# Optimization experiments

Hardware: AMD Instinct MI355X
Metric: run time of the kernel (lower is better)

The kernel has to match this reference:

```python
import jax, jax.numpy as jnp
import numpy as np

NEG_INF = -jnp.inf


def setup_inputs() -> dict:
    key = jax.random.key(0)
    ks = jax.random.split(key, 20)
    B, N, M = 8, 1024, 128
    F_OP, F_MA, F_E, OUT, HID = 64, 64, 16, 64, 128
    inp = {
        "x": jax.random.normal(ks[0], (B, N, F_OP), dtype=jnp.float32),
        "y": jax.random.normal(ks[1], (B, M, F_MA), dtype=jnp.float32),
        "z": jax.random.normal(ks[2], (B, N, M, F_E), dtype=jnp.float32),
        "op_adj_in": jax.random.randint(ks[3], (B, N, N), 0, 2, dtype=jnp.int32),
        "ma_adj_in": jax.random.randint(ks[4], (B, N, N), 0, 2, dtype=jnp.int32),
        "op_ma_adj": jax.random.randint(ks[5], (B, N, M), 0, 2, dtype=jnp.int32),
        # learned parameters
        "weight_op": jax.random.normal(ks[6], (F_OP, OUT), dtype=jnp.float32) * 0.1,
        "weight_ma": jax.random.normal(ks[7], (F_MA, OUT), dtype=jnp.float32) * 0.1,
        "weight_edge": jax.random.normal(ks[8], (F_E, OUT), dtype=jnp.float32) * 0.1,
        "attention_op": jax.random.normal(ks[9], (1, 2 * OUT), dtype=jnp.float32) * 0.1,
        "attention_ma": jax.random.normal(ks[10], (1, 3 * OUT), dtype=jnp.float32) * 0.1,
        "w1": jax.random.normal(ks[11], (2 * OUT, HID), dtype=jnp.float32) * 0.1,
        "b1": jnp.zeros((HID,), dtype=jnp.float32),
        "w2": jax.random.normal(ks[12], (HID, HID), dtype=jnp.float32) * 0.1,
        "b2": jnp.zeros((HID,), dtype=jnp.float32),
        "wo": jax.random.normal(ks[13], (HID, OUT), dtype=jnp.float32) * 0.1,
        "bo": jnp.zeros((OUT,), dtype=jnp.float32),
    }
    return inp


def reference(x, y, z, op_adj_in, ma_adj_in, op_ma_adj,
              weight_op, weight_ma, weight_edge, attention_op, attention_ma,
              w1, b1, w2, b2, wo, bo):
    OUT = weight_op.shape[1]
    h = jnp.einsum('bni,io->bno', x, weight_op)  # [B,N,OUT]
    # all_combinations[b,i,j] = cat(h[b,j], h[b,i]); dot with attention_op splits:
    a1 = attention_op[0, :OUT]
    a2 = attention_op[0, OUT:]
    e_op = (h @ a2)[:, :, None] + (h @ a1)[:, None, :]  # [B,N,N]
    e_op = jax.nn.leaky_relu(e_op, negative_slope=0.01)

    adj = (jnp.swapaxes(op_adj_in, 1, 2) + op_adj_in
           + jnp.swapaxes(ma_adj_in, 1, 2) + ma_adj_in)  # [B,N,N]
    row_mask = jnp.all(op_ma_adj == 0, axis=-1)  # [B,N] ops with no machine link
    adj = jnp.where(row_mask[:, :, None], 1, adj)
    att = jnp.where(adj > 0, e_op, NEG_INF)
    attention_in_op = jax.nn.softmax(att, axis=2)
    h_prime_op = jnp.einsum('bij,bjo->bio', attention_in_op, h)  # [B,N,OUT]

    h_ma = jnp.einsum('bmi,io->bmo', y, weight_ma)  # [B,M,OUT]
    h_edge = jnp.einsum('bnmi,io->bnmo', z, weight_edge)  # [B,N,M,OUT]
    # cat([h_op_i, h_ma_j, h_edge_ij]) @ attention_ma split into three dots
    am1 = attention_ma[0, :OUT]
    am2 = attention_ma[0, OUT:2 * OUT]
    am3 = attention_ma[0, 2 * OUT:]
    e_ma = (h @ am1)[:, :, None] + (h_ma @ am2)[:, None, :] + h_edge @ am3  # [B,N,M]
    e_ma = jax.nn.leaky_relu(e_ma, negative_slope=0.01)

    adj2 = jnp.where(row_mask[:, :, None], 1, op_ma_adj)
    att2 = jnp.where(adj2 > 0, e_ma, NEG_INF)
    attention_in_ma = jax.nn.softmax(att2, axis=2)  # [B,N,M]
    h_ma_edge = h_ma[:, None, :, :] + h_edge  # [B,N,M,OUT]
    h_prime_ma = jnp.einsum('bnm,bnmo->bno', attention_in_ma, h_ma_edge) + h

    h_prime = jnp.concatenate([h_prime_op, h_prime_ma], axis=-1)  # [B,N,2*OUT]
    embed = jax.nn.elu(h_prime @ w1 + b1)
    embed = jax.nn.elu(embed @ w2 + b2)
    embed = embed @ wo + bo
    embed = jnp.where(row_mask[:, :, None], 0.0, embed)
    return embed
```

## Files before the change

### kernel.cpp

```cpp
#include <hip/hip_runtime.h>
#include <math.h>

#define BB 8
#define NN 1024
#define MM 128
#define FOUT 64
#define HIDN 128

#define OFF_H       0
#define OFF_HMA     524288
#define OFF_HA1     589824
#define OFF_HA2     598016
#define OFF_HAM1    606208
#define OFF_HMAAM2  614400
#define OFF_RMASK   615424
#define OFF_WAM3    623616
#define OFF_HPRIME  623632
#define OFF_RDIR    1672208
#define OFF_OPMB    1934352
#define OFF_WT1HI   1967120
#define OFF_WT1LO   1975312
#define OFF_WT2HI   1983504
#define OFF_WT2LO   1991696
#define OFF_WTOHI   1999888
#define OFF_WTOLO   2003984
#define OFF_HTHI    2008080
#define OFF_HTLO    2270224
#define OFF_HMATHI  2532368
#define OFF_HMATLO  2565136
#define OFF_TRM     2597904

typedef __attribute__((ext_vector_type(8))) short bf16x8;
typedef __attribute__((ext_vector_type(8))) unsigned short u16x8;
typedef __attribute__((ext_vector_type(4))) float f32x4;

__device__ __forceinline__ void splitbf(float v, unsigned short& h, unsigned short& l) {
    unsigned u = __float_as_uint(v);
    unsigned hb = (u + 0x7FFFu + ((u >> 16) & 1u)) >> 16;
    float hf = __uint_as_float(hb << 16);
    float lf = v - hf;
    unsigned ul = __float_as_uint(lf);
    unsigned lb = (ul + 0x7FFFu + ((ul >> 16) & 1u)) >> 16;
    h = (unsigned short)hb; l = (unsigned short)lb;
}

__device__ __forceinline__ unsigned short tobf(float v) {
    unsigned u = __float_as_uint(v);
    return (unsigned short)((u + 0x7FFFu + ((u >> 16) & 1u)) >> 16);
}

__global__ __launch_bounds__(256) void k1_prep(
    const float* __restrict__ x, const float* __restrict__ y,
    const int* __restrict__ op_ma_adj,
    const int* __restrict__ op_adj, const int* __restrict__ ma_adj,
    const float* __restrict__ w_op, const float* __restrict__ w_ma,
    const float* __restrict__ w_edge,
    const float* __restrict__ att_op, const float* __restrict__ att_ma,
    const float* __restrict__ w1_g, const float* __restrict__ w2_g,
    const float* __restrict__ wo_g,
    float* __restrict__ h, float* __restrict__ h_ma,
    float* __restrict__ ha1, float* __restrict__ ha2, float* __restrict__ ham1,
    float* __restrict__ hmaam2, int* __restrict__ rmask, float* __restrict__ wam3,
    unsigned long long* __restrict__ rowdir, unsigned long long* __restrict__ opmb,
    unsigned short* __restrict__ trm,
    unsigned short* __restrict__ wt1hi, unsigned short* __restrict__ wt1lo,
    unsigned short* __restrict__ wt2hi, unsigned short* __restrict__ wt2lo,
    unsigned short* __restrict__ wtohi, unsigned short* __restrict__ wtolo,
    unsigned short* __restrict__ hthi, unsigned short* __restrict__ htlo,
    unsigned short* __restrict__ hmathi, unsigned short* __restrict__ hmatlo)
{
    __shared__ float wlds[64 * 64];
    __shared__ unsigned hstage[8 * 64];
    int bid = blockIdx.x;
    int t = threadIdx.x;
    int lane = t & 63;
    int wv = t >> 6;

    if (bid < 1024) {
        int b = bid >> 7;
        int n0g = (bid & 127) * 8;
        for (int k = t; k < 4096; k += 256) wlds[k] = w_op[k];
        float a1c = att_op[lane], a2c = att_op[64 + lane], am1c = att_ma[lane];
        __syncthreads();
        #pragma unroll
        for (int p = 0; p < 2; ++p) {
            int row = b * NN + n0g + p * 4 + wv;
            float xv = x[(size_t)row * 64 + lane];
            float acc0 = 0.f, acc1 = 0.f, acc2 = 0.f, acc3 = 0.f;
            #pragma unroll
            for (int i = 0; i < 16; ++i) {
                acc0 += __shfl(xv, i)      * wlds[i * 64 + lane];
                acc1 += __shfl(xv, i + 16) * wlds[(i + 16) * 64 + lane];
                acc2 += __shfl(xv, i + 32) * wlds[(i + 32) * 64 + lane];
                acc3 += __shfl(xv, i + 48) * wlds[(i + 48) * 64 + lane];
            }
            float acc = (acc0 + acc1) + (acc2 + acc3);
            h[(size_t)row * 64 + lane] = acc;
            unsigned short hs, ls;
            splitbf(acc, hs, ls);
            hstage[(p * 4 + wv) * 64 + lane] = (unsigned)hs | ((unsigned)ls << 16);
            float d1 = acc * a1c, d2 = acc * a2c, d3 = acc * am1c;
            #pragma unroll
            for (int m = 32; m; m >>= 1) {
                d1 += __shfl_xor(d1, m);
                d2 += __shfl_xor(d2, m);
                d3 += __shfl_xor(d3, m);
            }
            int v0 = op_ma_adj[(size_t)row * 128 + lane];
            int v1 = op_ma_adj[(size_t)row * 128 + 64 + lane];
            unsigned long long w0 = __ballot(v0 != 0);
            unsigned long long w1 = __ballot(v1 != 0);
            if (lane == 0) {
                ha1[row] = d1; ha2[row] = d2; ham1[row] = d3;
                opmb[row * 2] = w0; opmb[row * 2 + 1] = w1;
                rmask[row] = ((w0 | w1) == 0ULL) ? 1 : 0;
            }
        }
        __syncthreads();
        if (t < 128) {
            int o = t & 63;
            int plane = t >> 6;
            int sh = plane * 16;
            unsigned short* dst = plane ? htlo : hthi;
            u16x8 pk;
            #pragma unroll
            for (int k = 0; k < 8; ++k)
                pk[k] = (unsigned short)((hstage[k * 64 + o] >> sh) & 0xFFFFu);
            *(u16x8*)&dst[((size_t)(b * 64 + o)) * 1024 + n0g] = pk;
        }
    } else if (bid < 1152) {
        int bb = (bid - 1024) >> 4;
        int m0 = ((bid - 1024) & 15) * 8;
        for (int k = t; k < 4096; k += 256) wlds[k] = w_ma[k];
        float am2c = att_ma[64 + lane];
        __syncthreads();
        #pragma unroll
        for (int p = 0; p < 2; ++p) {
            int row = bb * MM + m0 + p * 4 + wv;
            float yv = y[(size_t)row * 64 + lane];
            float acc0 = 0.f, acc1 = 0.f, acc2 = 0.f, acc3 = 0.f;
            #pragma unroll
            for (int i = 0; i < 16; ++i) {
                acc0 += __shfl(yv, i)      * wlds[i * 64 + lane];
                acc1 += __shfl(yv, i + 16) * wlds[(i + 16) * 64 + lane];
                acc2 += __shfl(yv, i + 32) * wlds[(i + 32) * 64 + lane];
                acc3 += __shfl(yv, i + 48) * wlds[(i + 48) * 64 + lane];
            }
            float acc = (acc0 + acc1) + (acc2 + acc3);
            h_ma[(size_t)row * 64 + lane] = acc;
            unsigned short hs, ls;
            splitbf(acc, hs, ls);
            hstage[(p * 4 + wv) * 64 + lane] = (unsigned)hs | ((unsigned)ls << 16);
            float d = acc * am2c;
            #pragma unroll
            for (int m = 32; m; m >>= 1) d += __shfl_xor(d, m);
            if (lane == 0) hmaam2[row] = d;
        }
        __syncthreads();
        if (t < 128) {
            int o = t & 63;
            int plane = t >> 6;
            int sh = plane * 16;
            unsigned short* dst = plane ? hmatlo : hmathi;
            u16x8 pk;
            #pragma unroll
            for (int k = 0; k < 8; ++k)
                pk[k] = (unsigned short)((hstage[k * 64 + o] >> sh) & 0xFFFFu);
            *(u16x8*)&dst[((size_t)(bb * 64 + o)) * 128 + m0] = pk;
        }
    } else if (bid == 1152) {
        if (t < 16) {
            float s = 0.f;
            for (int o = 0; o < 64; ++o) s += w_edge[t * 64 + o] * att_ma[128 + o];
            wam3[t] = s;
        }
    } else if (bid < 3201) {
        unsigned char (*nib)[4][64] = (unsigned char(*)[4][64])wlds;
        int p = bid - 1153;
        int b = p >> 8;
        int rg = p & 255;
        int rl = t >> 6;
        int row = rg * 4 + rl;
        const int4* oprow = (const int4*)(op_adj + ((size_t)(b * NN + row)) * NN);
        const int4* marow = (const int4*)(ma_adj + ((size_t)(b * NN + row)) * NN);
        #pragma unroll
        for (int p2 = 0; p2 < 4; ++p2) {
            int4 vo = oprow[p2 * 64 + lane];
            int4 vm = marow[p2 * 64 + lane];
            unsigned nb = ((vo.x | vm.x) ? 1u : 0u) | ((vo.y | vm.y) ? 2u : 0u)
                        | ((vo.z | vm.z) ? 4u : 0u) | ((vo.w | vm.w) ? 8u : 0u);
            nib[rl][p2][lane] = (unsigned char)nb;
        }
        __syncthreads();
        if (t < 64) {
            int arl = t >> 4, q = t & 15;
            const unsigned* nw = (const unsigned*)&nib[arl][q >> 2][(q & 3) * 16];
            unsigned long long w = 0;
            #pragma unroll
            for (int u = 0; u < 4; ++u) {
                unsigned v = nw[u];
                w |= (unsigned long long)(v & 0xFu)         << (16 * u);
                w |= (unsigned long long)((v >> 8) & 0xFu)  << (16 * u + 4);
                w |= (unsigned long long)((v >> 16) & 0xFu) << (16 * u + 8);
                w |= (unsigned long long)((v >> 24) & 0xFu) << (16 * u + 12);
            }
            int jrow = rg * 4 + arl;
            rowdir[((size_t)(b * NN + jrow)) * 16 + q] = w;
            #pragma unroll
            for (int s = 0; s < 4; ++s) {
                trm[((size_t)(b * 64 + q * 4 + s)) * 1024 + jrow] =
                    (unsigned short)((w >> (16 * s)) & 0xFFFFu);
            }
        }
    } else {
        float (*tls)[33] = (float(*)[33])wlds;
        int p = bid - 3201;
        const float* src; unsigned short *dhi, *dlo; int KD, CD, tI, tJ;
        if (p < 16)      { src = w1_g; dhi = wt1hi; dlo = wt1lo; KD = 128; CD = 128; tI = p >> 2; tJ = p & 3; }
        else if (p < 32) { src = w2_g; dhi = wt2hi; dlo = wt2lo; KD = 128; CD = 128; tI = (p-16) >> 2; tJ = (p-16) & 3; }
        else             { src = wo_g; dhi = wtohi; dlo = wtolo; KD = 128; CD = 64;  tI = (p-32) >> 1; tJ = (p-32) & 1; }
        int k0 = tI * 32, c0 = tJ * 32;
        #pragma unroll
        for (int it = 0; it < 4; ++it) {
            int r = (t >> 5) + it * 8;
            int c = t & 31;
            tls[r][c] = src[(size_t)(k0 + r) * CD + c0 + c];
        }
        __syncthreads();
        #pragma unroll
        for (int it = 0; it < 4; ++it) {
            int c = (t >> 5) + it * 8;
            int k = t & 31;
            unsigned short hs, ls;
            splitbf(tls[k][c], hs, ls);
            dhi[(size_t)(c0 + c) * KD + k0 + k] = hs;
            dlo[(size_t)(c0 + c) * KD + k0 + k] = ls;
        }
    }
}

__global__ __launch_bounds__(256) void k2_opatt(
    const unsigned long long* __restrict__ rowdir,
    const unsigned short* __restrict__ trm,
    const unsigned short* __restrict__ hthi,
    const float* __restrict__ ha1, const float* __restrict__ ha2,
    const int* __restrict__ rmask, float* __restrict__ h_prime)
{
    __shared__ __align__(16) unsigned short Pl[8 * 1024];
    __shared__ float ha1s[1024];
    __shared__ unsigned long long dirw[8][16];
    __shared__ unsigned short trw[1024];
    __shared__ float rdeninv[8];
    int bid = blockIdx.x;
    int b = bid >> 7;
    int i0 = (bid & 127) << 3;
    int t = threadIdx.x;

    if (t < 128) {
        int rr = t >> 4, ww = t & 15;
        dirw[rr][ww] = rowdir[((size_t)(b * NN + i0 + rr)) * 16 + ww];
    }
    {
        const unsigned* src = (const unsigned*)(trm + ((size_t)(b * 64 + (i0 >> 4))) * 1024);
        ((unsigned*)trw)[t] = src[t];
        ((unsigned*)trw)[t + 256] = src[t + 256];
    }
    ha1s[t] = ha1[b * NN + t];
    ha1s[t + 256] = ha1[b * NN + t + 256];
    ha1s[t + 512] = ha1[b * NN + t + 512];
    ha1s[t + 768] = ha1[b * NN + t + 768];
    __syncthreads();

    int shbase = i0 & 8;

    {
        int row = t >> 5, q = t & 31;
        int bn = b * NN + i0 + row;
        float ha2i = ha2[bn];
        unsigned rmf = rmask[bn] ? 1u : 0u;

        float mh = -INFINITY;
        #pragma unroll 8
        for (int jj = 0; jj < 32; ++jj) {
            int j = q + (jj << 5);
            unsigned bit = ((unsigned)(dirw[row][jj >> 1] >> (q + ((jj & 1) << 5))) & 1u)
                         | ((unsigned)(trw[j] >> (shbase + row)) & 1u) | rmf;
            if (bit) mh = fmaxf(mh, ha1s[j]);
        }
        #pragma unroll
        for (int m = 1; m < 32; m <<= 1) mh = fmaxf(mh, __shfl_xor(mh, m));
        float mx = ha2i + mh;
        mx = mx > 0.f ? mx : 0.01f * mx;

        float s = 0.f;
        #pragma unroll 4
        for (int jj = 0; jj < 32; ++jj) {
            int j = q + (jj << 5);
            float ev = ha2i + ha1s[j];
            ev = ev > 0.f ? ev : 0.01f * ev;
            unsigned bit = ((unsigned)(dirw[row][jj >> 1] >> (q + ((jj & 1) << 5))) & 1u)
                         | ((unsigned)(trw[j] >> (shbase + row)) & 1u) | rmf;
            float u = bit ? __expf(ev - mx) : 0.f;
            s += u;
            unsigned short pb = tobf(u);
            unsigned byteoff = ((unsigned)(row * 2048 + j * 2)) ^ ((unsigned)(row << 4));
            *(unsigned short*)((char*)Pl + byteoff) = pb;
        }
        #pragma unroll
        for (int m = 1; m < 32; m <<= 1) s += __shfl_xor(s, m);
        if (q == 0) rdeninv[row] = 1.f / s;
    }
    __syncthreads();

    {
        int lane = t & 63, wvv = t >> 6;
        int arow = lane & 15, kg = lane >> 4;
        int prow = arow & 7;
        int col = wvv * 16 + arow;
        const unsigned short* bhp = hthi + ((size_t)(b * 64 + col)) * 1024;
        f32x4 acc = {0.f, 0.f, 0.f, 0.f};
        #pragma unroll 8
        for (int kst = 0; kst < 32; ++kst) {
            unsigned cc = ((unsigned)(kst * 4 + kg)) ^ ((unsigned)prow);
            bf16x8 pa = *(const bf16x8*)((char*)Pl + prow * 2048 + cc * 16);
            bf16x8 vh = *(const bf16x8*)&bhp[kst * 32 + kg * 8];
            acc = __builtin_amdgcn_mfma_f32_16x16x32_bf16(pa, vh, acc, 0, 0, 0);
        }
        if (kg < 2) {
            size_t base = (size_t)(b * NN + i0);
            #pragma unroll
            for (int r = 0; r < 4; ++r) {
                int orow = kg * 4 + r;
                float v = acc[r] * rdeninv[orow];
                h_prime[(base + orow) * 128 + col] = v;
            }
        }
    }
}

__global__ __launch_bounds__(256) void k3_maatt(
    const float* __restrict__ z, const unsigned long long* __restrict__ opmb,
    const float* __restrict__ h,
    const unsigned short* __restrict__ hmathi,
    const float* __restrict__ ham1, const float* __restrict__ hmaam2,
    const int* __restrict__ rmask, const float* __restrict__ wam3,
    const float* __restrict__ w_edge, float* __restrict__ h_prime)
{
    __shared__ __align__(16) unsigned short U_lds[4 * 136];
    __shared__ float wedge_s[1024];
    __shared__ float wam3s[16];
    __shared__ float zsum_s[4][16];
    __shared__ float rdeninv[4];

    int bid = blockIdx.x;
    int b = bid >> 8;
    int n0 = (bid & 255) * 4;
    int t = threadIdx.x;
    int lane = t & 63;
    int wv = t >> 6;

    for (int k = t; k < 1024; k += 256) wedge_s[k] = w_edge[k];
    if (t < 16) wam3s[t] = wam3[t];
    __syncthreads();

    {
        int bn = b * NN + n0 + wv;
        const float4* zr = (const float4*)(z + (size_t)bn * MM * 16);
        float4 a0 = zr[lane * 4 + 0];
        float4 a1 = zr[lane * 4 + 1];
        float4 a2 = zr[lane * 4 + 2];
        float4 a3 = zr[lane * 4 + 3];
        float4 c0 = zr[(lane + 64) * 4 + 0];
        float4 c1 = zr[(lane + 64) * 4 + 1];
        float4 c2 = zr[(lane + 64) * 4 + 2];
        float4 c3 = zr[(lane + 64) * 4 + 3];

        float hm0 = hmaam2[b * MM + lane];
        float hm1 = hmaam2[b * MM + 64 + lane];
        float base = ham1[bn];
        float e0 = base + hm0;
        float e1 = base + hm1;
        e0 += a0.x*wam3s[0] + a0.y*wam3s[1] + a0.z*wam3s[2] + a0.w*wam3s[3]
            + a1.x*wam3s[4] + a1.y*wam3s[5] + a1.z*wam3s[6] + a1.w*wam3s[7]
            + a2.x*wam3s[8] + a2.y*wam3s[9] + a2.z*wam3s[10] + a2.w*wam3s[11]
            + a3.x*wam3s[12] + a3.y*wam3s[13] + a3.z*wam3s[14] + a3.w*wam3s[15];
        e1 += c0.x*wam3s[0] + c0.y*wam3s[1] + c0.z*wam3s[2] + c0.w*wam3s[3]
            + c1.x*wam3s[4] + c1.y*wam3s[5] + c1.z*wam3s[6] + c1.w*wam3s[7]
            + c2.x*wam3s[8] + c2.y*wam3s[9] + c2.z*wam3s[10] + c2.w*wam3s[11]
            + c3.x*wam3s[12] + c3.y*wam3s[13] + c3.z*wam3s[14] + c3.w*wam3s[15];
        e0 = e0 > 0.f ? e0 : 0.01f * e0;
        e1 = e1 > 0.f ? e1 : 0.01f * e1;
        unsigned long long bits0 = opmb[(size_t)bn * 2];
        unsigned long long bits1 = opmb[(size_t)bn * 2 + 1];
        int rm = rmask[bn];
        int v0 = rm | (int)((bits0 >> lane) & 1ULL);
        int v1 = rm | (int)((bits1 >> lane) & 1ULL);
        e0 = v0 ? e0 : -INFINITY;
        e1 = v1 ? e1 : -INFINITY;

        float mx = fmaxf(e0, e1);
        #pragma unroll
        for (int msk = 32; msk; msk >>= 1) mx = fmaxf(mx, __shfl_xor(mx, msk));
        float u0 = __expf(e0 - mx);
        float u1 = __expf(e1 - mx);
        float s = u0 + u1;
        #pragma unroll
        for (int msk = 32; msk; msk >>= 1) s += __shfl_xor(s, msk);

        U_lds[wv * 136 + lane] = tobf(u0);
        U_lds[wv * 136 + 64 + lane] = tobf(u1);
        if (lane == 0) rdeninv[wv] = 1.f / s;

        float zv[16];
        zv[0]=u0*a0.x+u1*c0.x;  zv[1]=u0*a0.y+u1*c0.y;
        zv[2]=u0*a0.z+u1*c0.z;  zv[3]=u0*a0.w+u1*c0.w;
        zv[4]=u0*a1.x+u1*c1.x;  zv[5]=u0*a1.y+u1*c1.y;
        zv[6]=u0*a1.z+u1*c1.z;  zv[7]=u0*a1.w+u1*c1.w;
        zv[8]=u0*a2.x+u1*c2.x;  zv[9]=u0*a2.y+u1*c2.y;
        zv[10]=u0*a2.z+u1*c2.z; zv[11]=u0*a2.w+u1*c2.w;
        zv[12]=u0*a3.x+u1*c3.x; zv[13]=u0*a3.y+u1*c3.y;
        zv[14]=u0*a3.z+u1*c3.z; zv[15]=u0*a3.w+u1*c3.w;
        #pragma unroll
        for (int s2 = 0; s2 < 8; ++s2) {
            float sel = (lane & 1) ? zv[s2] : zv[s2 + 8];
            float got = __shfl_xor(sel, 1);
            zv[s2] = ((lane & 1) ? zv[s2 + 8] : zv[s2]) + got;
        }
        #pragma unroll
        for (int s2 = 0; s2 < 4; ++s2) {
            float sel = (lane & 2) ? zv[s2] : zv[s2 + 4];
            float got = __shfl_xor(sel, 2);
            zv[s2] = ((lane & 2) ? zv[s2 + 4] : zv[s2]) + got;
        }
        #pragma unroll
        for (int s2 = 0; s2 < 2; ++s2) {
            float sel = (lane & 4) ? zv[s2] : zv[s2 + 2];
            float got = __shfl_xor(sel, 4);
            zv[s2] = ((lane & 4) ? zv[s2 + 2] : zv[s2]) + got;
        }
        {
            float sel = (lane & 8) ? zv[0] : zv[1];
            float got = __shfl_xor(sel, 8);
            zv[0] = ((lane & 8) ? zv[1] : zv[0]) + got;
        }
        zv[0] += __shfl_xor(zv[0], 16);
        zv[0] += __shfl_xor(zv[0], 32);
        if (lane < 16) {
            int comp = ((lane & 1) << 3) | ((lane & 2) << 1) | ((lane & 4) >> 1) | ((lane & 8) >> 3);
            zsum_s[wv][comp] = zv[0];
        }
    }
    __syncthreads();

    {
        int arow = lane & 15, kg = lane >> 4;
        int col = wv * 16 + arow;
        bf16x8 ua[4];
        #pragma unroll
        for (int ks = 0; ks < 4; ++ks)
            ua[ks] = *(const bf16x8*)&U_lds[(arow & 3) * 136 + kg * 8 + ks * 32];
        const unsigned short* bhp = hmathi + ((size_t)(b * 64 + col)) * 128 + kg * 8;
        f32x4 acc = {0.f, 0.f, 0.f, 0.f};
        #pragma unroll
        for (int ks = 0; ks < 4; ++ks) {
            bf16x8 bh = *(const bf16x8*)&bhp[ks * 32];
            acc = __builtin_amdgcn_mfma_f32_16x16x32_bf16(ua[ks], bh, acc, 0, 0, 0);
        }
        if (kg == 0) {
            #pragma unroll
            for (int r = 0; r < 4; ++r) {
                float he = 0.f;
                #pragma unroll
                for (int i = 0; i < 16; ++i) he += zsum_s[r][i] * wedge_s[i * 64 + col];
                int bn = b * NN + n0 + r;
                float val = (acc[r] + he) * rdeninv[r] + h[(size_t)bn * 64 + col];
                h_prime[(size_t)bn * 128 + 64 + col] = val;
            }
        }
    }
}

__global__ __launch_bounds__(256) void k4_mlp(
    const float* __restrict__ hp, const int* __restrict__ rmask,
    const unsigned short* __restrict__ wt1hi, const unsigned short* __restrict__ wt1lo,
    const unsigned short* __restrict__ wt2hi, const unsigned short* __restrict__ wt2lo,
    const unsigned short* __restrict__ wtohi, const unsigned short* __restrict__ wtolo,
    const float* __restrict__ b1, const float* __restrict__ b2,
    const float* __restrict__ bo, float* __restrict__ out)
{
    __shared__ __align__(16) unsigned short Ahi0[16 * 136];
    __shared__ __align__(16) unsigned short Alo0[16 * 136];
    __shared__ __align__(16) unsigned short Ahi1[16 * 136];
    __shared__ __align__(16) unsigned short Alo1[16 * 136];
    __shared__ __align__(16) unsigned short Whi[64 * 128];
    __shared__ __align__(16) unsigned short Wlo[64 * 128];
    __shared__ int rml[16];
    int t = threadIdx.x;
    int lane = t & 63;
    int wv = t >> 6;
    int row0 = blockIdx.x * 16;
    int plane = t >> 7;
    int q = t & 127;

    {
        int r = t >> 4;
        int cg = (t & 15) * 8;
        const float* src = hp + (size_t)(row0 + r) * 128 + cg;
        float4 v0 = *(const float4*)src;
        float4 v1 = *(const float4*)(src + 4);
        float xs[8] = {v0.x, v0.y, v0.z, v0.w, v1.x, v1.y, v1.z, v1.w};
        u16x8 hv, lv;
        #pragma unroll
        for (int j = 0; j < 8; ++j) {
            unsigned short hs, ls;
            splitbf(xs[j], hs, ls);
            hv[j] = hs; lv[j] = ls;
        }
        *(u16x8*)&Ahi0[r * 136 + cg] = hv;
        *(u16x8*)&Alo0[r * 136 + cg] = lv;
        if (t < 16) rml[t] = rmask[row0 + t];
    }
    __syncthreads();

    int arow = lane & 15;
    int kg = lane >> 4;
    int aoff = arow * 136 + kg * 8;
    int lcol = wv * 16 + arow;

    {
        bf16x8 ah[4], al[4];
        #pragma unroll
        for (int ks = 0; ks < 4; ++ks) {
            ah[ks] = *(const bf16x8*)&Ahi0[aoff + ks * 32];
            al[ks] = *(const bf16x8*)&Alo0[aoff + ks * 32];
        }
        #pragma unroll
        for (int half = 0; half < 2; ++half) {
            __syncthreads();
            {
                const unsigned short* gsrc = plane ? wt1lo : wt1hi;
                char* dst = (char*)(plane ? Wlo : Whi);
                #pragma unroll
                for (int i = 0; i < 8; ++i) {
                    int L = q * 8 + i;
                    int col = L >> 4, kc = L & 15;
                    u16x8 v = *(const u16x8*)&gsrc[(size_t)(half * 64 + col) * 128 + kc * 8];
                    unsigned byteoff = ((unsigned)(col * 256 + kc * 16)) ^ ((unsigned)((col & 7) << 4));
                    *(u16x8*)(dst + byteoff) = v;
                }
            }
            __syncthreads();
            int col = half * 64 + lcol;
            f32x4 acc = {0.f, 0.f, 0.f, 0.f};
            #pragma unroll
            for (int ks = 0; ks < 4; ++ks) {
                unsigned wb = ((unsigned)(lcol * 256 + kg * 16 + ks * 64)) ^ ((unsigned)((arow & 7) << 4));
                bf16x8 bh = *(const bf16x8*)((char*)Whi + wb);
                bf16x8 bl = *(const bf16x8*)((char*)Wlo + wb);
                acc = __builtin_amdgcn_mfma_f32_16x16x32_bf16(ah[ks], bh, acc, 0, 0, 0);
                acc = __builtin_amdgcn_mfma_f32_16x16x32_bf16(al[ks], bh, acc, 0, 0, 0);
                acc = __builtin_amdgcn_mfma_f32_16x16x32_bf16(ah[ks], bl, acc, 0, 0, 0);
            }
            float bb = b1[col];
            #pragma unroll
            for (int r = 0; r < 4; ++r) {
                int row = kg * 4 + r;
                float v = acc[r] + bb;
                v = v > 0.f ? v : __expf(v) - 1.f;
                unsigned short hs, ls;
                splitbf(v, hs, ls);
                Ahi1[row * 136 + col] = hs;
                Alo1[row * 136 + col] = ls;
            }
        }
    }
    __syncthreads();

    {
        bf16x8 ah[4], al[4];
        #pragma unroll
        for (int ks = 0; ks < 4; ++ks) {
            ah[ks] = *(const bf16x8*)&Ahi1[aoff + ks * 32];
            al[ks] = *(const bf16x8*)&Alo1[aoff + ks * 32];
        }
        #pragma unroll
        for (int half = 0; half < 2; ++half) {
            __syncthreads();
            {
                const unsigned short* gsrc = plane ? wt2lo : wt2hi;
                char* dst = (char*)(plane ? Wlo : Whi);
                #pragma unroll
                for (int i = 0; i < 8; ++i) {
                    int L = q * 8 + i;
                    int col = L >> 4, kc = L & 15;
                    u16x8 v = *(const u16x8*)&gsrc[(size_t)(half * 64 + col) * 128 + kc * 8];
                    unsigned byteoff = ((unsigned)(col * 256 + kc * 16)) ^ ((unsigned)((col & 7) << 4));
                    *(u16x8*)(dst + byteoff) = v;
                }
            }
            __syncthreads();
            int col = half * 64 + lcol;
            f32x4 acc = {0.f, 0.f, 0.f, 0.f};
            #pragma unroll
            for (int ks = 0; ks < 4; ++ks) {
                unsigned wb = ((unsigned)(lcol * 256 + kg * 16 + ks * 64)) ^ ((unsigned)((arow & 7) << 4));
                bf16x8 bh = *(const bf16x8*)((char*)Whi + wb);
                bf16x8 bl = *(const bf16x8*)((char*)Wlo + wb);
                acc = __builtin_amdgcn_mfma_f32_16x16x32_bf16(ah[ks], bh, acc, 0, 0, 0);
                acc = __builtin_amdgcn_mfma_f32_16x16x32_bf16(al[ks], bh, acc, 0, 0, 0);
                acc = __builtin_amdgcn_mfma_f32_16x16x32_bf16(ah[ks], bl, acc, 0, 0, 0);
            }
            float bb = b2[col];
            #pragma unroll
            for (int r = 0; r < 4; ++r) {
                int row = kg * 4 + r;
                float v = acc[r] + bb;
                v = v > 0.f ? v : __expf(v) - 1.f;
                unsigned short hs, ls;
                splitbf(v, hs, ls);
                Ahi0[row * 136 + col] = hs;
                Alo0[row * 136 + col] = ls;
            }
        }
    }
    __syncthreads();

    {
        bf16x8 ah[4], al[4];
        #pragma unroll
        for (int ks = 0; ks < 4; ++ks) {
            ah[ks] = *(const bf16x8*)&Ahi0[aoff + ks * 32];
            al[ks] = *(const bf16x8*)&Alo0[aoff + ks * 32];
        }
        __syncthreads();
        {
            const unsigned short* gsrc = plane ? wtolo : wtohi;
            char* dst = (char*)(plane ? Wlo : Whi);
            #pragma unroll
            for (int i = 0; i < 8; ++i) {
                int L = q * 8 + i;
                int col = L >> 4, kc = L & 15;
                u16x8 v = *(const u16x8*)&gsrc[(size_t)col * 128 + kc * 8];
                unsigned byteoff = ((unsigned)(col * 256 + kc * 16)) ^ ((unsigned)((col & 7) << 4));
                *(u16x8*)(dst + byteoff) = v;
            }
        }
        __syncthreads();
        int col = lcol;
        f32x4 acc = {0.f, 0.f, 0.f, 0.f};
        #pragma unroll
        for (int ks = 0; ks < 4; ++ks) {
            unsigned wb = ((unsigned)(lcol * 256 + kg * 16 + ks * 64)) ^ ((unsigned)((arow & 7) << 4));
            bf16x8 bh = *(const bf16x8*)((char*)Whi + wb);
            bf16x8 bl = *(const bf16x8*)((char*)Wlo + wb);
            acc = __builtin_amdgcn_mfma_f32_16x16x32_bf16(ah[ks], bh, acc, 0, 0, 0);
            acc = __builtin_amdgcn_mfma_f32_16x16x32_bf16(al[ks], bh, acc, 0, 0, 0);
            acc = __builtin_amdgcn_mfma_f32_16x16x32_bf16(ah[ks], bl, acc, 0, 0, 0);
        }
        float bb = bo[col];
        #pragma unroll
        for (int r = 0; r < 4; ++r) {
            int row = kg * 4 + r;
            float v = acc[r] + bb;
            out[(size_t)(row0 + row) * 64 + col] = rml[row] ? 0.f : v;
        }
    }
}

extern "C" void kernel_launch(void* const* d_in, const int* in_sizes, int n_in,
                              void* d_out, int out_size, void* d_ws, size_t ws_size,
                              hipStream_t stream) {
    const float* x      = (const float*)d_in[0];
    const float* y      = (const float*)d_in[1];
    const float* z      = (const float*)d_in[2];
    const int*   op_adj = (const int*)d_in[3];
    const int*   ma_adj = (const int*)d_in[4];
    const int*   opma   = (const int*)d_in[5];
    const float* w_op   = (const float*)d_in[6];
    const float* w_ma   = (const float*)d_in[7];
    const float* w_edge = (const float*)d_in[8];
    const float* att_op = (const float*)d_in[9];
    const float* att_ma = (const float*)d_in[10];
    const float* w1     = (const float*)d_in[11];
    const float* b1     = (const float*)d_in[12];
    const float* w2     = (const float*)d_in[13];
    const float* b2     = (const float*)d_in[14];
    const float* wo     = (const float*)d_in[15];
    const float* bo     = (const float*)d_in[16];
    float* out = (float*)d_out;

    float* ws = (float*)d_ws;
    float* h       = ws + OFF_H;
    float* h_ma    = ws + OFF_HMA;
    float* ha1     = ws + OFF_HA1;
    float* ha2     = ws + OFF_HA2;
    float* ham1    = ws + OFF_HAM1;
    float* hmaam2  = ws + OFF_HMAAM2;
    int*   rmask   = (int*)(ws + OFF_RMASK);
    float* wam3    = ws + OFF_WAM3;
    float* h_prime = ws + OFF_HPRIME;
    unsigned long long* rowdir = (unsigned long long*)(ws + OFF_RDIR);
    unsigned long long* opmb = (unsigned long long*)(ws + OFF_OPMB);
    unsigned short* trm   = (unsigned short*)(ws + OFF_TRM);
    unsigned short* wt1hi = (unsigned short*)(ws + OFF_WT1HI);
    unsigned short* wt1lo = (unsigned short*)(ws + OFF_WT1LO);
    unsigned short* wt2hi = (unsigned short*)(ws + OFF_WT2HI);
    unsigned short* wt2lo = (unsigned short*)(ws + OFF_WT2LO);
    unsigned short* wtohi = (unsigned short*)(ws + OFF_WTOHI);
    unsigned short* wtolo = (unsigned short*)(ws + OFF_WTOLO);
    unsigned short* hthi  = (unsigned short*)(ws + OFF_HTHI);
    unsigned short* htlo  = (unsigned short*)(ws + OFF_HTLO);
    unsigned short* hmathi = (unsigned short*)(ws + OFF_HMATHI);
    unsigned short* hmatlo = (unsigned short*)(ws + OFF_HMATLO);

    k1_prep<<<1024 + 128 + 1 + 2048 + 40, 256, 0, stream>>>(
        x, y, opma, op_adj, ma_adj, w_op, w_ma, w_edge, att_op, att_ma,
        w1, w2, wo,
        h, h_ma, ha1, ha2, ham1, hmaam2, rmask, wam3, rowdir, opmb, trm,
        wt1hi, wt1lo, wt2hi, wt2lo, wtohi, wtolo, hthi, htlo, hmathi, hmatlo);

    k2_opatt<<<1024, 256, 0, stream>>>(
        rowdir, trm, hthi, ha1, ha2, rmask, h_prime);

    k3_maatt<<<2048, 256, 0, stream>>>(
        z, opmb, h, hmathi, ham1, hmaam2, rmask, wam3, w_edge, h_prime);

    k4_mlp<<<512, 256, 0, stream>>>(
        h_prime, rmask, wt1hi, wt1lo, wt2hi, wt2lo, wtohi, wtolo,
        b1, b2, bo, out);
}
```

Baseline: 84.40 us.

## Merge op and machine attention kernels into one launch, replace masked max with global max

Combines the op-attention and machine-attention kernels into a single 3072-block launch that branches on block index, so the two independent stages share one launch and can run concurrently. The op-attention softmax now uses the unmasked maximum of ha1 across the whole row, computed by a block reduction, in place of the masked per-row max loop, which drops one pass over the 1024 columns. Using a looser max stays valid for softmax, but it may underflow exp when masked-in values sit far below the global max. The merged kernel also carries the union of both shared-memory footprints, which can lower occupancy for both halves.

```diff
diff --git a/kernel.cpp b/kernel.cpp
--- a/kernel.cpp
+++ b/kernel.cpp
@@ -239,106 +239,11 @@
     }
 }
 
-__global__ __launch_bounds__(256) void k2_opatt(
+__global__ __launch_bounds__(256) void k23_att(
     const unsigned long long* __restrict__ rowdir,
     const unsigned short* __restrict__ trm,
     const unsigned short* __restrict__ hthi,
     const float* __restrict__ ha1, const float* __restrict__ ha2,
-    const int* __restrict__ rmask, float* __restrict__ h_prime)
-{
-    __shared__ __align__(16) unsigned short Pl[8 * 1024];
-    __shared__ float ha1s[1024];
-    __shared__ unsigned long long dirw[8][16];
-    __shared__ unsigned short trw[1024];
-    __shared__ float rdeninv[8];
-    int bid = blockIdx.x;
-    int b = bid >> 7;
-    int i0 = (bid & 127) << 3;
-    int t = threadIdx.x;
-
-    if (t < 128) {
-        int rr = t >> 4, ww = t & 15;
-        dirw[rr][ww] = rowdir[((size_t)(b * NN + i0 + rr)) * 16 + ww];
-    }
-    {
-        const unsigned* src = (const unsigned*)(trm + ((size_t)(b * 64 + (i0 >> 4))) * 1024);
-        ((unsigned*)trw)[t] = src[t];
-        ((unsigned*)trw)[t + 256] = src[t + 256];
-    }
-    ha1s[t] = ha1[b * NN + t];
-    ha1s[t + 256] = ha1[b * NN + t + 256];
-    ha1s[t + 512] = ha1[b * NN + t + 512];
-    ha1s[t + 768] = ha1[b * NN + t + 768];
-    __syncthreads();
-
-    int shbase = i0 & 8;
-
-    {
-        int row = t >> 5, q = t & 31;
-        int bn = b * NN + i0 + row;
-        float ha2i = ha2[bn];
-        unsigned rmf = rmask[bn] ? 1u : 0u;
-
-        float mh = -INFINITY;
-        #pragma unroll 8
-        for (int jj = 0; jj < 32; ++jj) {
-            int j = q + (jj << 5);
-            unsigned bit = ((unsigned)(dirw[row][jj >> 1] >> (q + ((jj & 1) << 5))) & 1u)
-                         | ((unsigned)(trw[j] >> (shbase + row)) & 1u) | rmf;
-            if (bit) mh = fmaxf(mh, ha1s[j]);
-        }
-        #pragma unroll
-        for (int m = 1; m < 32; m <<= 1) mh = fmaxf(mh, __shfl_xor(mh, m));
-        float mx = ha2i + mh;
-        mx = mx > 0.f ? mx : 0.01f * mx;
-
-        float s = 0.f;
-        #pragma unroll 4
-        for (int jj = 0; jj < 32; ++jj) {
-            int j = q + (jj << 5);
-            float ev = ha2i + ha1s[j];
-            ev = ev > 0.f ? ev : 0.01f * ev;
-            unsigned bit = ((unsigned)(dirw[row][jj >> 1] >> (q + ((jj & 1) << 5))) & 1u)
-                         | ((unsigned)(trw[j] >> (shbase + row)) & 1u) | rmf;
-            float u = bit ? __expf(ev - mx) : 0.f;
-            s += u;
-            unsigned short pb = tobf(u);
-            unsigned byteoff = ((unsigned)(row * 2048 + j * 2)) ^ ((unsigned)(row << 4));
-            *(unsigned short*)((char*)Pl + byteoff) = pb;
-        }
-        #pragma unroll
-        for (int m = 1; m < 32; m <<= 1) s += __shfl_xor(s, m);
-        if (q == 0) rdeninv[row] = 1.f / s;
-    }
-    __syncthreads();
-
-    {
-        int lane = t & 63, wvv = t >> 6;
-        int arow = lane & 15, kg = lane >> 4;
-        int prow = arow & 7;
-        int col = wvv * 16 + arow;
-        const unsigned short* bhp = hthi + ((size_t)(b * 64 + col)) * 1024;
-        f32x4 acc = {0.f, 0.f, 0.f, 0.f};
-        #pragma unroll 8
-        for (int kst = 0; kst < 32; ++kst) {
-            unsigned cc = ((unsigned)(kst * 4 + kg)) ^ ((unsigned)prow);
-            bf16x8 pa = *(const bf16x8*)((char*)Pl + prow * 2048 + cc * 16);
-            bf16x8 vh = *(const bf16x8*)&bhp[kst * 32 + kg * 8];
-            acc = __builtin_amdgcn_mfma_f32_16x16x32_bf16(pa, vh, acc, 0, 0, 0);
-        }
-        if (kg < 2) {
-            size_t base = (size_t)(b * NN + i0);
-            #pragma unroll
-            for (int r = 0; r < 4; ++r) {
-                int orow = kg * 4 + r;
-                float v = acc[r] * rdeninv[orow];
-                h_prime[(base + orow) * 128 + col] = v;
-            }
-        }
-    }
-}
-
-__global__ __launch_bounds__(256) void k3_maatt(
     const float* __restrict__ z, const unsigned long long* __restrict__ opmb,
     const float* __restrict__ h,
     const unsigned short* __restrict__ hmathi,
@@ -346,18 +251,107 @@
     const int* __restrict__ rmask, const float* __restrict__ wam3,
     const float* __restrict__ w_edge, float* __restrict__ h_prime)
 {
+    __shared__ __align__(16) unsigned short Pl[8 * 1024];
+    __shared__ float ha1s[1024];
+    __shared__ unsigned long long dirw[8][16];
+    __shared__ unsigned short trw[1024];
+    __shared__ float rdeninv8[8];
+    __shared__ float wmx[4];
     __shared__ __align__(16) unsigned short U_lds[4 * 136];
     __shared__ float wedge_s[1024];
     __shared__ float wam3s[16];
     __shared__ float zsum_s[4][16];
-    __shared__ float rdeninv[4];
-
-    int bid = blockIdx.x;
-    int b = bid >> 8;
-    int n0 = (bid & 255) * 4;
+    __shared__ float rdeninv4[4];
+
     int t = threadIdx.x;
     int lane = t & 63;
     int wv = t >> 6;
+
+    if (blockIdx.x < 1024) {
+        int bid = blockIdx.x;
+        int b = bid >> 7;
+        int i0 = (bid & 127) << 3;
+
+        if (t < 128) {
+            int rr = t >> 4, ww = t & 15;
+            dirw[rr][ww] = rowdir[((size_t)(b * NN + i0 + rr)) * 16 + ww];
+        }
+        {
+            const unsigned* src = (const unsigned*)(trm + ((size_t)(b * 64 + (i0 >> 4))) * 1024);
+            ((unsigned*)trw)[t] = src[t];
+            ((unsigned*)trw)[t + 256] = src[t + 256];
+        }
+        float v0 = ha1[b * NN + t];
+        float v1 = ha1[b * NN + t + 256];
+        float v2 = ha1[b * NN + t + 512];
+        float v3 = ha1[b * NN + t + 768];
+        ha1s[t] = v0; ha1s[t + 256] = v1; ha1s[t + 512] = v2; ha1s[t + 768] = v3;
+        float m4 = fmaxf(fmaxf(v0, v1), fmaxf(v2, v3));
+        #pragma unroll
+        for (int m = 1; m < 64; m <<= 1) m4 = fmaxf(m4, __shfl_xor(m4, m));
+        if (lane == 0) wmx[wv] = m4;
+        __syncthreads();
+        float mhall = fmaxf(fmaxf(wmx[0], wmx[1]), fmaxf(wmx[2], wmx[3]));
+
+        int shbase = i0 & 8;
+
+        {
+            int row = t >> 5, q = t & 31;
+            int bn = b * NN + i0 + row;
+            float ha2i = ha2[bn];
+            unsigned rmf = rmask[bn] ? 1u : 0u;
+            float mx = ha2i + mhall;
+            mx = mx > 0.f ? mx : 0.01f * mx;
+
+            float s = 0.f;
+            #pragma unroll 4
+            for (int jj = 0; jj < 32; ++jj) {
+                int j = q + (jj << 5);
+                float ev = ha2i + ha1s[j];
+                ev = ev > 0.f ? ev : 0.01f * ev;
+                unsigned bit = ((unsigned)(dirw[row][jj >> 1] >> (q + ((jj & 1) << 5))) & 1u)
+                             | ((unsigned)(trw[j] >> (shbase + row)) & 1u) | rmf;
+                float u = bit ? __expf(ev - mx) : 0.f;
+                s += u;
+                unsigned short pb = tobf(u);
+                unsigned byteoff = ((unsigned)(row * 2048 + j * 2)) ^ ((unsigned)(row << 4));
+                *(unsigned short*)((char*)Pl + byteoff) = pb;
+            }
+            #pragma unroll
+            for (int m = 1; m < 32; m <<= 1) s += __shfl_xor(s, m);
+            if (q == 0) rdeninv8[row] = 1.f / s;
+        }
+        __syncthreads();
+
+        {
+            int arow = lane & 15, kg = lane >> 4;
+            int prow = arow & 7;
+            int col = wv * 16 + arow;
+            const unsigned short* bhp = hthi + ((size_t)(b * 64 + col)) * 1024;
+            f32x4 acc = {0.f, 0.f, 0.f, 0.f};
+            #pragma unroll 8
+            for (int kst = 0; kst < 32; ++kst) {
+                unsigned cc = ((unsigned)(kst * 4 + kg)) ^ ((unsigned)prow);
+                bf16x8 pa = *(const bf16x8*)((char*)Pl + prow * 2048 + cc * 16);
+                bf16x8 vh = *(const bf16x8*)&bhp[kst * 32 + kg * 8];
+                acc = __builtin_amdgcn_mfma_f32_16x16x32_bf16(pa, vh, acc, 0, 0, 0);
+            }
+            if (kg < 2) {
+                size_t base = (size_t)(b * NN + i0);
+                #pragma unroll
+                for (int r = 0; r < 4; ++r) {
+                    int orow = kg * 4 + r;
+                    float v = acc[r] * rdeninv8[orow];
+                    h_prime[(base + orow) * 128 + col] = v;
+                }
+            }
+        }
+        return;
+    }
+
+    int bid = blockIdx.x - 1024;
+    int b = bid >> 8;
+    int n0 = (bid & 255) * 4;
 
     for (int k = t; k < 1024; k += 256) wedge_s[k] = w_edge[k];
     if (t < 16) wam3s[t] = wam3[t];
@@ -409,7 +403,7 @@
 
         U_lds[wv * 136 + lane] = tobf(u0);
         U_lds[wv * 136 + 64 + lane] = tobf(u1);
-        if (lane == 0) rdeninv[wv] = 1.f / s;
+        if (lane == 0) rdeninv4[wv] = 1.f / s;
 
         float zv[16];
         zv[0]=u0*a0.x+u1*c0.x;  zv[1]=u0*a0.y+u1*c0.y;
@@ -473,7 +467,7 @@
                 #pragma unroll
                 for (int i = 0; i < 16; ++i) he += zsum_s[r][i] * wedge_s[i * 64 + col];
                 int bn = b * NN + n0 + r;
-                float val = (acc[r] + he) * rdeninv[r] + h[(size_t)bn * 64 + col];
+                float val = (acc[r] + he) * rdeninv4[r] + h[(size_t)bn * 64 + col];
                 h_prime[(size_t)bn * 128 + 64 + col] = val;
             }
         }
@@ -719,10 +713,8 @@
         h, h_ma, ha1, ha2, ham1, hmaam2, rmask, wam3, rowdir, opmb, trm,
         wt1hi, wt1lo, wt2hi, wt2lo, wtohi, wtolo, hthi, htlo, hmathi, hmatlo);
 
-    k2_opatt<<<1024, 256, 0, stream>>>(
-        rowdir, trm, hthi, ha1, ha2, rmask, h_prime);
-
-    k3_maatt<<<2048, 256, 0, stream>>>(
+    k23_att<<<3072, 256, 0, stream>>>(
+        rowdir, trm, hthi, ha1, ha2,
         z, opmb, h, hmathi, ham1, hmaam2, rmask, wam3, w_edge, h_prime);
 
     k4_mlp<<<512, 256, 0, stream>>>(
```

Measured after the change: 78.48 us. 7.0% less time.
